# Performance work log

Hardware: AMD Instinct MI355X
Metric: run time of the kernel (lower is better)

Reference implementation:

```python
import jax, jax.numpy as jnp
import numpy as np

H = 1024   # hidden_dim
L = 2      # n_layers
V = 512    # dict_size['target']
B = 256    # batch
S = 512    # encoder seq len
IN = 64    # maxlen['input'][0] = encoder input feature dim
T = 64     # maxlen['target'] = decoder steps


def setup_inputs() -> dict:
    key = jax.random.key(0)
    ks = jax.random.split(key, 16)
    def p(k, shape):
        return jax.random.normal(k, shape, jnp.float32) * 0.05
    emb = p(ks[0], (V, H)).at[0].set(0.0)  # padding_idx=0 row is zero
    return dict(
        x=jax.random.normal(ks[1], (B, S, IN), jnp.float32),
        emb=emb,
        enc_Wih0=p(ks[2], (3 * H, IN)), enc_Whh0=p(ks[3], (3 * H, H)),
        enc_bih0=p(ks[4], (3 * H,)),   enc_bhh0=p(ks[5], (3 * H,)),
        enc_Wih1=p(ks[6], (3 * H, H)), enc_Whh1=p(ks[7], (3 * H, H)),
        enc_bih1=p(ks[8], (3 * H,)),   enc_bhh1=p(ks[9], (3 * H,)),
        dec_Wih=p(ks[10], (L, 3 * H, H)), dec_Whh=p(ks[11], (L, 3 * H, H)),
        dec_bih=p(ks[12], (L, 3 * H)),    dec_bhh=p(ks[13], (L, 3 * H)),
        fc_W=p(ks[14], (V, H)), fc_b=p(ks[15], (V,)),
    )


def gru_cell(x, h, Wih, Whh, bih, bhh):
    # torch GRU cell: r,z,n gate ordering
    gx = x @ Wih.T + bih            # (B, 3H)
    gh = h @ Whh.T + bhh            # (B, 3H)
    rx, zx, nx = jnp.split(gx, 3, axis=-1)
    rh, zh, nh = jnp.split(gh, 3, axis=-1)
    r = jax.nn.sigmoid(rx + rh)
    z = jax.nn.sigmoid(zx + zh)
    n = jnp.tanh(nx + r * nh)
    return (1.0 - z) * n + z * h


def reference(x, emb, enc_Wih0, enc_Whh0, enc_bih0, enc_bhh0,
              enc_Wih1, enc_Whh1, enc_bih1, enc_bhh1,
              dec_Wih, dec_Whh, dec_bih, dec_bhh, fc_W, fc_b):
    b = x.shape[0]
    # ---------- encoder: 2-layer unidirectional GRU ----------
    seq = jnp.swapaxes(x, 0, 1)  # (S, B, IN) time-major for scan
    enc_params = [(enc_Wih0, enc_Whh0, enc_bih0, enc_bhh0),
                  (enc_Wih1, enc_Whh1, enc_bih1, enc_bhh1)]
    finals = []
    for (Wih, Whh, bih, bhh) in enc_params:
        h0 = jnp.zeros((b, H), seq.dtype)
        def step(h, xt, Wih=Wih, Whh=Whh, bih=bih, bhh=bhh):
            hn = gru_cell(xt, h, Wih, Whh, bih, bhh)
            return hn, hn
        hT, seq = jax.lax.scan(step, h0, seq)
        finals.append(hT)
    hidden = jnp.stack(finals)  # (L, B, H)

    tok0 = jnp.zeros((b,), jnp.int32)  # start token 0 (== <pad>)

    def dec_step(carry, _):
        hcur, tok = carry
        inp = emb[tok]                       # (B, H) embedding lookup
        new_h = []
        for l in range(L):
            hn = gru_cell(inp, hcur[l], dec_Wih[l], dec_Whh[l],
                          dec_bih[l], dec_bhh[l])
            new_h.append(hn)
            inp = hn
        logits = inp @ fc_W.T + fc_b         # (B, V)
        tok = jnp.argmax(logits, axis=-1).astype(jnp.int32)
        return (jnp.stack(new_h), tok), logits

    (h_fin, _), logits_seq = jax.lax.scan(dec_step, (hidden, tok0), None, length=T)
    out = jnp.swapaxes(logits_seq, 0, 1)     # (B, T, V)
    return out, h_fin
```

## Files before the change

### kernel.cpp

```cpp
#include <hip/hip_runtime.h>
#include <math.h>

namespace {

constexpr int BSZ = 256;
constexpr int SEQ = 512;
constexpr int KIN = 64;
constexpr int HID = 1024;
constexpr int GD  = 3072;
constexpr int VOC = 512;
constexpr int TT  = 64;

typedef _Float16 half_t;
typedef _Float16 half8 __attribute__((ext_vector_type(8)));
typedef float f32x4 __attribute__((ext_vector_type(4)));

constexpr float LOSCL = 4096.f;
constexpr float LOINV = 1.f / 4096.f;

__device__ __forceinline__ void decode_mc(int bb, int& m0, int& c0) {
  int c_lo = bb & 7, rest = bb >> 3;
  int m = rest & 7, c_hi = rest >> 3;
  m0 = m * 32;
  c0 = (c_hi * 8 + c_lo) * 32;
}

__global__ __launch_bounds__(256) void swz_kernel(
    const float* __restrict__ src, half_t* __restrict__ hi,
    half_t* __restrict__ lo, int NG, int NKCH, int HIDR, int n)
{
  int i = blockIdx.x * 256 + threadIdx.x;
  if (i >= n) return;
  int j = i & 7, l = (i >> 3) & 63;
  int frag = i >> 9;
  int g = frag % NG;
  int rest = frag / NG;
  int w4 = rest & 3;
  int rest2 = rest >> 2;
  int kc = rest2 % NKCH;
  int ct = rest2 / NKCH;
  int ldw = NKCH * 64;
  int row = g * HIDR + ct * 32 + (w4 & 1) * 16 + (l & 15);
  int col = kc * 64 + (w4 >> 1) * 32 + (l >> 4) * 8 + j;
  float f = src[(size_t)row * ldw + col];
  half_t h = (half_t)f;
  hi[i] = h;
  lo[i] = (half_t)((f - (float)h) * LOSCL);
}

typedef half_t AldsT[2][2][32][136];

template<int NG, int G2>
__device__ __forceinline__ void gemm_swz128(
    const float* __restrict__ A, size_t lda, int nch,
    const half_t* __restrict__ Whi, const half_t* __restrict__ Wlo,
    int ct, int kc0, int nkch_tot, int m0,
    f32x4 (&aH)[4][2], f32x4 (&aL)[4][2], AldsT& Alds)
{
  const int tid = threadIdx.x;
  const int wv = tid >> 6, l = tid & 63, lr = l & 15, lk = l >> 4;
  const int colg = wv & 1, ksg = wv >> 1;
  const int arow = tid >> 3, aseg = tid & 7;
  const float* aptr = A + (size_t)(m0 + arow) * lda + aseg * 16;

  const size_t FR = (size_t)NG * 512;
  const size_t S2STR = 2 * FR;
  const size_t CSTR = 8 * FR;
  const size_t bbase =
      (((size_t)(ct * nkch_tot + kc0 + ksg)) * 4 + colg) * FR + l * 8;
  const half_t* bph = Whi + bbase;
  const half_t* bpl = Wlo + bbase;

  float4 paE[4], paO[4];
  half8 bhE[2 * NG], blE[2 * NG], bhO[2 * NG], blO[2 * NG];
  #pragma unroll
  for (int q = 0; q < 4; ++q) paE[q] = *(const float4*)(aptr + q * 4);
  #pragma unroll
  for (int s2 = 0; s2 < 2; ++s2)
    #pragma unroll
    for (int g = 0; g < NG; ++g) {
      bhE[s2 * NG + g] = *(const half8*)(bph + s2 * S2STR + g * 512);
      blE[s2 * NG + g] = *(const half8*)(bpl + s2 * S2STR + g * 512);
    }

#define SWC(pac, bhc, blc, pan, bhn, bln, CH, BUF)                            \
  {                                                                           \
    {               \
      float vals[16] = {pac[0].x, pac[0].y, pac[0].z, pac[0].w,               \
                        pac[1].x, pac[1].y, pac[1].z, pac[1].w,               \
                        pac[2].x, pac[2].y, pac[2].z, pac[2].w,               \
                        pac[3].x, pac[3].y, pac[3].z, pac[3].w};              \
      half8 hi8[2], lo8[2];                                                   \
      _Pragma("unroll") for (int j = 0; j < 16; ++j) {                        \
        float f = vals[j]; half_t h = (half_t)f;                              \
        hi8[j >> 3][j & 7] = h;                                               \
        lo8[j >> 3][j & 7] = (half_t)((f - (float)h) * LOSCL);                \
      }                                                                       \
      *(half8*)&Alds[BUF][0][arow][aseg * 16] = hi8[0];                       \
      *(half8*)&Alds[BUF][0][arow][aseg * 16 + 8] = hi8[1];                   \
      *(half8*)&Alds[BUF][1][arow][aseg * 16] = lo8[0];                       \
      *(half8*)&Alds[BUF][1][arow][aseg * 16 + 8] = lo8[1];                   \
    }                                                                         \
    __syncthreads();                                                          \
    if ((CH) + 1 < nch) {                                                     \
      _Pragma("unroll") for (int q = 0; q < 4; ++q)                           \
        pan[q] = *(const float4*)(aptr + ((CH) + 1) * 128 + q * 4);           \
      _Pragma("unroll") for (int s2 = 0; s2 < 2; ++s2)                        \
        _Pragma("unroll") for (int g = 0; g < NG; ++g) {                      \
          bhn[s2 * NG + g] =                                                  \
              *(const half8*)(bph + ((CH) + 1) * CSTR + s2 * S2STR + g * 512);\
          bln[s2 * NG + g] =                                                  \
              *(const half8*)(bpl + ((CH) + 1) * CSTR + s2 * S2STR + g * 512);\
        }                                                                     \
    }                                                                         \
    _Pragma("unroll") for (int s2 = 0; s2 < 2; ++s2) {                        \
      half8 ah0 = *(const half8*)&Alds[BUF][0][lr][ksg * 64 + s2 * 32 + lk * 8];      \
      half8 ah1 = *(const half8*)&Alds[BUF][0][16 + lr][ksg * 64 + s2 * 32 + lk * 8]; \
      half8 al0 = *(const half8*)&Alds[BUF][1][lr][ksg * 64 + s2 * 32 + lk * 8];      \
      half8 al1 = *(const half8*)&Alds[BUF][1][16 + lr][ksg * 64 + s2 * 32 + lk * 8]; \
      _Pragma("unroll") for (int g = 0; g < NG; ++g) {                        \
        const int slot = (g == 2) ? G2 : g;                                   \
        half8 bh = bhc[s2 * NG + g];                                          \
        half8 bl = blc[s2 * NG + g];                                          \
        aH[slot][0] = __builtin_amdgcn_mfma_f32_16x16x32_f16(ah0, bh, aH[slot][0], 0, 0, 0); \
        aH[slot][1] = __builtin_amdgcn_mfma_f32_16x16x32_f16(ah1, bh, aH[slot][1], 0, 0, 0); \
        aL[slot][0] = __builtin_amdgcn_mfma_f32_16x16x32_f16(ah0, bl, aL[slot][0], 0, 0, 0); \
        aL[slot][0] = __builtin_amdgcn_mfma_f32_16x16x32_f16(al0, bh, aL[slot][0], 0, 0, 0); \
        aL[slot][1] = __builtin_amdgcn_mfma_f32_16x16x32_f16(ah1, bl, aL[slot][1], 0, 0, 0); \
        aL[slot][1] = __builtin_amdgcn_mfma_f32_16x16x32_f16(al1, bh, aL[slot][1], 0, 0, 0); \
      }                                                                       \
    }                                                                         \
  }

  for (int ch = 0; ch < nch; ch += 2) {
    SWC(paE, bhE, blE, paO, bhO, blO, ch, 0)
    SWC(paO, bhO, blO, paE, bhE, blE, (ch + 1), 1)
  }
#undef SWC
}

template<int NG, int G2>
__device__ __forceinline__ void gemm_swz64(
    const float* __restrict__ A, size_t lda,
    const half_t* __restrict__ Whi, const half_t* __restrict__ Wlo,
    int ct, int nkch_tot, int m0,
    f32x4 (&aH)[4][2], f32x4 (&aL)[4][2], AldsT& Alds)
{
  const int tid = threadIdx.x;
  const int wv = tid >> 6, l = tid & 63, lr = l & 15, lk = l >> 4;
  const int colg = wv & 1, ksg = wv >> 1;
  const int arow = tid >> 3, aseg = tid & 7;
  const float* aptr = A + (size_t)(m0 + arow) * lda + aseg * 8;

  const size_t FR = (size_t)NG * 512;
  const size_t bbase =
      (((size_t)(ct * nkch_tot)) * 4 + (colg + 2 * ksg)) * FR + l * 8;
  half8 bh[NG], bl[NG];
  #pragma unroll
  for (int g = 0; g < NG; ++g) {
    bh[g] = *(const half8*)(Whi + bbase + g * 512);
    bl[g] = *(const half8*)(Wlo + bbase + g * 512);
  }
  float4 u0 = *(const float4*)(aptr);
  float4 u1 = *(const float4*)(aptr + 4);
  {
    float vals[8] = {u0.x, u0.y, u0.z, u0.w, u1.x, u1.y, u1.z, u1.w};
    half8 hi8, lo8;
    #pragma unroll
    for (int j = 0; j < 8; ++j) {
      float f = vals[j]; half_t h = (half_t)f;
      hi8[j] = h; lo8[j] = (half_t)((f - (float)h) * LOSCL);
    }
    *(half8*)&Alds[0][0][arow][aseg * 8] = hi8;
    *(half8*)&Alds[0][1][arow][aseg * 8] = lo8;
  }
  __syncthreads();
  half8 ah0 = *(const half8*)&Alds[0][0][lr][ksg * 32 + lk * 8];
  half8 ah1 = *(const half8*)&Alds[0][0][16 + lr][ksg * 32 + lk * 8];
  half8 al0 = *(const half8*)&Alds[0][1][lr][ksg * 32 + lk * 8];
  half8 al1 = *(const half8*)&Alds[0][1][16 + lr][ksg * 32 + lk * 8];
  #pragma unroll
  for (int g = 0; g < NG; ++g) {
    const int slot = (g == 2) ? G2 : g;
    aH[slot][0] = __builtin_amdgcn_mfma_f32_16x16x32_f16(ah0, bh[g], aH[slot][0], 0, 0, 0);
    aH[slot][1] = __builtin_amdgcn_mfma_f32_16x16x32_f16(ah1, bh[g], aH[slot][1], 0, 0, 0);
    aL[slot][0] = __builtin_amdgcn_mfma_f32_16x16x32_f16(ah0, bl[g], aL[slot][0], 0, 0, 0);
    aL[slot][0] = __builtin_amdgcn_mfma_f32_16x16x32_f16(al0, bh[g], aL[slot][0], 0, 0, 0);
    aL[slot][1] = __builtin_amdgcn_mfma_f32_16x16x32_f16(ah1, bl[g], aL[slot][1], 0, 0, 0);
    aL[slot][1] = __builtin_amdgcn_mfma_f32_16x16x32_f16(al1, bh[g], aL[slot][1], 0, 0, 0);
  }
}

template<int NS>
__device__ __forceinline__ void combine_ks(
    f32x4 (&aH)[4][2], f32x4 (&aL)[4][2], float* __restrict__ xch)
{
  const int tid = threadIdx.x;
  const int wv = tid >> 6, l = tid & 63;
  const int colg = wv & 1, ksg = wv >> 1;
  #pragma unroll
  for (int q = 0; q < NS; ++q)
    #pragma unroll
    for (int mf = 0; mf < 2; ++mf)
      aH[q][mf] = aH[q][mf] + aL[q][mf] * LOINV;
  __syncthreads();
  float* base = xch + ((size_t)colg * 64 + l) * (NS * 8);
  if (ksg == 1) {
    #pragma unroll
    for (int q = 0; q < NS; ++q)
      #pragma unroll
      for (int mf = 0; mf < 2; ++mf)
        *(f32x4*)(base + q * 8 + mf * 4) = aH[q][mf];
  }
  __syncthreads();
  if (ksg == 0) {
    #pragma unroll
    for (int q = 0; q < NS; ++q)
      #pragma unroll
      for (int mf = 0; mf < 2; ++mf)
        aH[q][mf] = aH[q][mf] + *(const f32x4*)(base + q * 8 + mf * 4);
  }
}

__device__ __forceinline__ void gru_epi32(
    f32x4 (&vv)[4][2],
    const float* __restrict__ bih, const float* __restrict__ bhh,
    const float* __restrict__ hprev, float* __restrict__ hout,
    int m0, int c0)
{
  const int tid = threadIdx.x;
  if (tid >= 128) return;
  const int wv = tid >> 6, l = tid & 63, lr = l & 15, lk = l >> 4;
  const int c = c0 + (wv & 1) * 16 + lr;
  float bhr = bhh[c], bhz = bhh[HID + c], bhn = bhh[2 * HID + c];
  float bir = 0.f, biz = 0.f, bin = 0.f;
  if (bih) { bir = bih[c]; biz = bih[HID + c]; bin = bih[2 * HID + c]; }
  #pragma unroll
  for (int mf = 0; mf < 2; ++mf) {
    #pragma unroll
    for (int i = 0; i < 4; ++i) {
      int b = m0 + mf * 16 + lk * 4 + i;
      float rs = vv[0][mf][i] + bhr + bir;
      float zs = vv[1][mf][i] + bhz + biz;
      float nx = vv[2][mf][i] + bin;
      float nh = vv[3][mf][i] + bhn;
      float r = 1.f / (1.f + expf(-rs));
      float z = 1.f / (1.f + expf(-zs));
      float n = tanhf(nx + r * nh);
      hout[(size_t)b * HID + c] =
          (1.f - z) * n + z * hprev[(size_t)b * HID + c];
    }
  }
}

__device__ __forceinline__ void write_partials32(
    f32x4 (&vv)[4][2], int s2, float* __restrict__ P, int m0, int c0)
{
  const int tid = threadIdx.x;
  if (tid >= 128) return;
  const int wv = tid >> 6, l = tid & 63, lr = l & 15, lk = l >> 4;
  const int c = c0 + (wv & 1) * 16 + lr;
  #pragma unroll
  for (int g = 0; g < 3; ++g) {
    const int slot = (g == 2) ? s2 : g;
    #pragma unroll
    for (int mf = 0; mf < 2; ++mf) {
      #pragma unroll
      for (int i = 0; i < 4; ++i) {
        int b = m0 + mf * 16 + lk * 4 + i;
        P[((size_t)g * BSZ + b) * HID + c] = vv[slot][mf][i];
      }
    }
  }
}

#define INIT_ACC(aH, aL)                                  \
  _Pragma("unroll") for (int q = 0; q < 4; ++q)           \
    _Pragma("unroll") for (int m_ = 0; m_ < 2; ++m_) {    \
      aH[q][m_] = (f32x4){0.f, 0.f, 0.f, 0.f};            \
      aL[q][m_] = (f32x4){0.f, 0.f, 0.f, 0.f};            \
    }

__global__ __launch_bounds__(256, 2) void enc_step_mfma(
    int s, const float* __restrict__ x,
    const half_t* __restrict__ Wih0h, const half_t* __restrict__ Wih0l,
    const float* __restrict__ bih0,
    const half_t* __restrict__ Whh0h, const half_t* __restrict__ Whh0l,
    const float* __restrict__ bhh0,
    const half_t* __restrict__ Wih1h, const half_t* __restrict__ Wih1l,
    const float* __restrict__ bih1,
    const half_t* __restrict__ Whh1h, const half_t* __restrict__ Whh1l,
    const float* __restrict__ bhh1,
    float* __restrict__ h0f, float* __restrict__ h1f)
{
  __shared__ __align__(16) AldsT Alds;
  f32x4 aH[4][2], aL[4][2];
  INIT_ACC(aH, aL)
  const size_t BH = (size_t)BSZ * HID;
  int blk = blockIdx.x;
  if (blk < 256) {
    if (s >= SEQ) return;
    int m0, c0; decode_mc(blk, m0, c0);
    int ct = c0 >> 5;
    const float* hp = h0f + ((s + 1) & 1) * BH;
    gemm_swz128<3, 3>(hp, HID, 8, Whh0h, Whh0l, ct, 0, 16, m0, aH, aL, Alds);
    gemm_swz64<3, 2>(x + (size_t)s * KIN, (size_t)SEQ * KIN, Wih0h, Wih0l,
                     ct, 1, m0, aH, aL, Alds);
    combine_ks<4>(aH, aL, (float*)Alds);
    gru_epi32(aH, bih0, bhh0, hp, h0f + (s & 1) * BH, m0, c0);
  } else {
    if (s < 1) return;
    int u = s - 1;
    int m0, c0; decode_mc(blk - 256, m0, c0);
    int ct = c0 >> 5;
    const float* hp = h1f + ((u + 1) & 1) * BH;
    const float* h0in = h0f + (u & 1) * BH;
    gemm_swz128<3, 3>(hp, HID, 8, Whh1h, Whh1l, ct, 0, 16, m0, aH, aL, Alds);
    gemm_swz128<3, 2>(h0in, HID, 8, Wih1h, Wih1l, ct, 0, 16, m0, aH, aL, Alds);
    combine_ks<4>(aH, aL, (float*)Alds);
    gru_epi32(aH, bih1, bhh1, hp, h1f + (u & 1) * BH, m0, c0);
  }
}

__global__ __launch_bounds__(256, 2) void gru0_main(
    const float* __restrict__ hprev,
    const half_t* __restrict__ Whhh, const half_t* __restrict__ Whhl,
    float* __restrict__ Pg)
{
  __shared__ __align__(16) AldsT Alds;
  f32x4 aH[4][2], aL[4][2];
  INIT_ACC(aH, aL)
  int bb = blockIdx.x;
  int kh = bb >> 8;
  int m0, c0; decode_mc(bb & 255, m0, c0);
  int ct = c0 >> 5;
  gemm_swz128<3, 3>(hprev + kh * 512, HID, 4, Whhh, Whhl, ct, kh * 8, 16, m0,
                    aH, aL, Alds);
  combine_ks<4>(aH, aL, (float*)Alds);
  write_partials32(aH, 3, Pg + (size_t)kh * 3 * BSZ * HID, m0, c0);
}

__global__ __launch_bounds__(256) void gru0_epi(
    const float* __restrict__ Pg, const float* __restrict__ bhh,
    const float* __restrict__ E, const int* __restrict__ tok,
    const float* __restrict__ hprev, float* __restrict__ hout)
{
  int idx = (blockIdx.x * 256 + threadIdx.x) * 4;
  int b = idx >> 10, c = idx & 1023;
  const size_t BH3 = (size_t)3 * BSZ * HID;
  float4 r0 = *(const float4*)&Pg[((size_t)0 * BSZ + b) * HID + c];
  float4 z0 = *(const float4*)&Pg[((size_t)1 * BSZ + b) * HID + c];
  float4 n0 = *(const float4*)&Pg[((size_t)2 * BSZ + b) * HID + c];
  float4 r1 = *(const float4*)&Pg[BH3 + ((size_t)0 * BSZ + b) * HID + c];
  float4 z1 = *(const float4*)&Pg[BH3 + ((size_t)1 * BSZ + b) * HID + c];
  float4 n1 = *(const float4*)&Pg[BH3 + ((size_t)2 * BSZ + b) * HID + c];
  const float* Er = E + (size_t)tok[b] * GD;
  float4 exr = *(const float4*)&Er[c];
  float4 exz = *(const float4*)&Er[HID + c];
  float4 exn = *(const float4*)&Er[2 * HID + c];
  float4 hp = *(const float4*)&hprev[(size_t)b * HID + c];
  float r0v[4] = {r0.x, r0.y, r0.z, r0.w}, z0v[4] = {z0.x, z0.y, z0.z, z0.w};
  float n0v[4] = {n0.x, n0.y, n0.z, n0.w}, r1v[4] = {r1.x, r1.y, r1.z, r1.w};
  float z1v[4] = {z1.x, z1.y, z1.z, z1.w}, n1v[4] = {n1.x, n1.y, n1.z, n1.w};
  float exrv[4] = {exr.x, exr.y, exr.z, exr.w};
  float exzv[4] = {exz.x, exz.y, exz.z, exz.w};
  float exnv[4] = {exn.x, exn.y, exn.z, exn.w};
  float hpv[4] = {hp.x, hp.y, hp.z, hp.w};
  float ov[4];
  #pragma unroll
  for (int j = 0; j < 4; ++j) {
    int cc = c + j;
    float rs = r0v[j] + r1v[j] + bhh[cc] + exrv[j];
    float zs = z0v[j] + z1v[j] + bhh[HID + cc] + exzv[j];
    float nh = n0v[j] + n1v[j] + bhh[2 * HID + cc];
    float r = 1.f / (1.f + expf(-rs));
    float z = 1.f / (1.f + expf(-zs));
    float n = tanhf(exnv[j] + r * nh);
    ov[j] = (1.f - z) * n + z * hpv[j];
  }
  float4 o; o.x = ov[0]; o.y = ov[1]; o.z = ov[2]; o.w = ov[3];
  *(float4*)&hout[(size_t)b * HID + c] = o;
}

__global__ __launch_bounds__(256, 2) void dec_l1_main(
    const float* __restrict__ hd1prev, const float* __restrict__ ho0,
    const half_t* __restrict__ Whhh, const half_t* __restrict__ Whhl,
    const half_t* __restrict__ Wihh, const half_t* __restrict__ Wihl,
    float* __restrict__ Phh, float* __restrict__ Pih)
{
  __shared__ __align__(16) AldsT Alds;
  f32x4 aH[4][2], aL[4][2];
  INIT_ACC(aH, aL)
  int bb = blockIdx.x;
  if (bb < 256) {
    int m0, c0; decode_mc(bb, m0, c0);
    gemm_swz128<3, 3>(hd1prev, HID, 8, Whhh, Whhl, c0 >> 5, 0, 16, m0,
                      aH, aL, Alds);
    combine_ks<4>(aH, aL, (float*)Alds);
    write_partials32(aH, 3, Phh, m0, c0);
  } else {
    int m0, c0; decode_mc(bb - 256, m0, c0);
    gemm_swz128<3, 2>(ho0, HID, 8, Wihh, Wihl, c0 >> 5, 0, 16, m0,
                      aH, aL, Alds);
    combine_ks<4>(aH, aL, (float*)Alds);
    write_partials32(aH, 2, Pih, m0, c0);
  }
}

__global__ __launch_bounds__(256) void dec_l1_epi(
    const float* __restrict__ Phh, const float* __restrict__ Pih,
    const float* __restrict__ bih, const float* __restrict__ bhh,
    const float* __restrict__ hprev, float* __restrict__ hout)
{
  int idx = (blockIdx.x * 256 + threadIdx.x) * 4;
  int b = idx >> 10, c = idx & 1023;
  float4 rh = *(const float4*)&Phh[((size_t)0 * BSZ + b) * HID + c];
  float4 zh = *(const float4*)&Phh[((size_t)1 * BSZ + b) * HID + c];
  float4 nh = *(const float4*)&Phh[((size_t)2 * BSZ + b) * HID + c];
  float4 rx = *(const float4*)&Pih[((size_t)0 * BSZ + b) * HID + c];
  float4 zx = *(const float4*)&Pih[((size_t)1 * BSZ + b) * HID + c];
  float4 nx = *(const float4*)&Pih[((size_t)2 * BSZ + b) * HID + c];
  float4 hp = *(const float4*)&hprev[(size_t)b * HID + c];
  float rhv[4] = {rh.x, rh.y, rh.z, rh.w}, zhv[4] = {zh.x, zh.y, zh.z, zh.w};
  float nhv[4] = {nh.x, nh.y, nh.z, nh.w}, rxv[4] = {rx.x, rx.y, rx.z, rx.w};
  float zxv[4] = {zx.x, zx.y, zx.z, zx.w}, nxv[4] = {nx.x, nx.y, nx.z, nx.w};
  float hpv[4] = {hp.x, hp.y, hp.z, hp.w};
  float ov[4];
  #pragma unroll
  for (int j = 0; j < 4; ++j) {
    int cc = c + j;
    float r = 1.f / (1.f + expf(-(rhv[j] + rxv[j] + bhh[cc] + bih[cc])));
    float z = 1.f / (1.f + expf(-(zhv[j] + zxv[j] + bhh[HID + cc] + bih[HID + cc])));
    float n = tanhf(nxv[j] + bih[2 * HID + cc] + r * (nhv[j] + bhh[2 * HID + cc]));
    ov[j] = (1.f - z) * n + z * hpv[j];
  }
  float4 o; o.x = ov[0]; o.y = ov[1]; o.z = ov[2]; o.w = ov[3];
  *(float4*)&hout[(size_t)b * HID + c] = o;
}

__global__ __launch_bounds__(256, 2) void fc_main(
    const float* __restrict__ h,
    const half_t* __restrict__ Wh, const half_t* __restrict__ Wl,
    float* __restrict__ Pfc)
{
  __shared__ __align__(16) AldsT Alds;
  f32x4 aH[4][2], aL[4][2];
  INIT_ACC(aH, aL)
  int bb = blockIdx.x;
  int kh = bb >> 7, sub = bb & 127;
  int v_lo = sub & 7, rest = sub >> 3;
  int m = rest & 7, v_hi = rest >> 3;
  int m0 = m * 32, v0 = (v_hi * 8 + v_lo) * 32;
  gemm_swz128<1, 0>(h + kh * 512, HID, 4, Wh, Wl, v0 >> 5, kh * 8, 16, m0,
                    aH, aL, Alds);
  combine_ks<1>(aH, aL, (float*)Alds);

  const int tid = threadIdx.x;
  if (tid >= 128) return;
  const int wv = tid >> 6, l = tid & 63, lr = l & 15, lk = l >> 4;
  int v = v0 + (wv & 1) * 16 + lr;
  float* P = Pfc + (size_t)kh * BSZ * VOC;
  #pragma unroll
  for (int mf = 0; mf < 2; ++mf) {
    #pragma unroll
    for (int i = 0; i < 4; ++i) {
      int b = m0 + mf * 16 + lk * 4 + i;
      P[(size_t)b * VOC + v] = aH[0][mf][i];
    }
  }
}

__global__ __launch_bounds__(256) void fc_epi(
    const float* __restrict__ Pfc, const float* __restrict__ fcb,
    float* __restrict__ out, int t, int* __restrict__ tok)
{
  __shared__ float sv[4];
  __shared__ int si[4];
  int b = blockIdx.x, tid = threadIdx.x;
  int va = tid, vb = tid + 256;
  float lga = Pfc[(size_t)b * VOC + va] + Pfc[((size_t)BSZ + b) * VOC + va] + fcb[va];
  float lgb = Pfc[(size_t)b * VOC + vb] + Pfc[((size_t)BSZ + b) * VOC + vb] + fcb[vb];
  out[((size_t)b * TT + t) * VOC + va] = lga;
  out[((size_t)b * TT + t) * VOC + vb] = lgb;
  float best = lga; int bi = va;
  if (lgb > best) { best = lgb; bi = vb; }
  #pragma unroll
  for (int off = 1; off < 64; off <<= 1) {
    float ov = __shfl_xor(best, off);
    int oi = __shfl_xor(bi, off);
    if (ov > best || (ov == best && oi < bi)) { best = ov; bi = oi; }
  }
  int wv = tid >> 6;
  if ((tid & 63) == 0) { sv[wv] = best; si[wv] = bi; }
  __syncthreads();
  if (tid == 0) {
    #pragma unroll
    for (int w = 1; w < 4; ++w)
      if (sv[w] > best || (sv[w] == best && si[w] < bi)) { best = sv[w]; bi = si[w]; }
    tok[b] = bi;
  }
}

__global__ __launch_bounds__(256) void e0_kernel(
    const float* __restrict__ emb, const float* __restrict__ Wih,
    const float* __restrict__ bih, float* __restrict__ E0)
{
  __shared__ float As[32][34];
  __shared__ float Bs[32][68];
  int m0 = (blockIdx.x & 15) << 5;
  int c0 = (blockIdx.x >> 4) << 6;
  int tid = threadIdx.x, tx = tid & 15, ty = tid >> 4;
  float acc[2][4] = {};
  for (int k0 = 0; k0 < HID; k0 += 32) {
    { int m = tid >> 3, kq = (tid & 7) << 2;
      float4 v = *(const float4*)(emb + (size_t)(m0 + m) * HID + k0 + kq);
      As[kq+0][m] = v.x; As[kq+1][m] = v.y; As[kq+2][m] = v.z; As[kq+3][m] = v.w; }
    #pragma unroll
    for (int r = 0; r < 2; ++r) {
      int idx = (r << 8) + tid;
      int n = idx >> 3, kq = (idx & 7) << 2;
      float4 v = *(const float4*)(Wih + (size_t)(c0 + n) * HID + k0 + kq);
      Bs[kq+0][n] = v.x; Bs[kq+1][n] = v.y; Bs[kq+2][n] = v.z; Bs[kq+3][n] = v.w;
    }
    __syncthreads();
    #pragma unroll 4
    for (int k = 0; k < 32; ++k) {
      float a0 = As[k][(ty << 1)], a1 = As[k][(ty << 1) + 1];
      float4 b = *(const float4*)&Bs[k][tx << 2];
      float bb[4] = {b.x, b.y, b.z, b.w};
      #pragma unroll
      for (int j = 0; j < 4; ++j) {
        acc[0][j] = fmaf(a0, bb[j], acc[0][j]);
        acc[1][j] = fmaf(a1, bb[j], acc[1][j]);
      }
    }
    __syncthreads();
  }
  #pragma unroll
  for (int i = 0; i < 2; ++i) {
    int v = m0 + (ty << 1) + i;
    #pragma unroll
    for (int j = 0; j < 4; ++j) {
      int g = c0 + (tx << 2) + j;
      E0[(size_t)v * GD + g] = acc[i][j] + bih[g];
    }
  }
}

}

extern "C" void kernel_launch(void* const* d_in, const int* in_sizes, int n_in,
                              void* d_out, int out_size, void* d_ws, size_t ws_size,
                              hipStream_t stream)
{
  const float* x     = (const float*)d_in[0];
  const float* emb   = (const float*)d_in[1];
  const float* eWih0 = (const float*)d_in[2];
  const float* eWhh0 = (const float*)d_in[3];
  const float* ebih0 = (const float*)d_in[4];
  const float* ebhh0 = (const float*)d_in[5];
  const float* eWih1 = (const float*)d_in[6];
  const float* eWhh1 = (const float*)d_in[7];
  const float* ebih1 = (const float*)d_in[8];
  const float* ebhh1 = (const float*)d_in[9];
  const float* dWih  = (const float*)d_in[10];
  const float* dWhh  = (const float*)d_in[11];
  const float* dbih  = (const float*)d_in[12];
  const float* dbhh  = (const float*)d_in[13];
  const float* fcW   = (const float*)d_in[14];
  const float* fcb   = (const float*)d_in[15];
  float* out = (float*)d_out;

  const size_t BH = (size_t)BSZ * HID;

  char* p = (char*)d_ws;
  auto alloc = [&](size_t bytes) {
    char* r = p; p += (bytes + 255) & ~(size_t)255; return r;
  };
  float* E0   = (float*)alloc((size_t)VOC * GD * 4);
  float* h0f  = (float*)alloc(2 * BH * 4);
  float* h1f  = (float*)alloc(2 * BH * 4);
  float* hd0f = (float*)alloc(2 * BH * 4);
  float* hd1f = (float*)alloc(2 * BH * 4);
  float* Phh  = (float*)alloc(3 * BH * 4);
  float* Pih  = (float*)alloc(3 * BH * 4);
  float* Pg   = (float*)alloc(6 * BH * 4);
  float* Pfc  = (float*)alloc((size_t)2 * BSZ * VOC * 4);
  const int NW_IH0 = GD * KIN, NW = GD * HID, NW_FC = VOC * HID;
  half_t* eWih0h = (half_t*)alloc((size_t)NW_IH0 * 2);
  half_t* eWih0l = (half_t*)alloc((size_t)NW_IH0 * 2);
  half_t* eWhh0h = (half_t*)alloc((size_t)NW * 2);
  half_t* eWhh0l = (half_t*)alloc((size_t)NW * 2);
  half_t* eWih1h = (half_t*)alloc((size_t)NW * 2);
  half_t* eWih1l = (half_t*)alloc((size_t)NW * 2);
  half_t* eWhh1h = (half_t*)alloc((size_t)NW * 2);
  half_t* eWhh1l = (half_t*)alloc((size_t)NW * 2);
  half_t* dWhh0h = (half_t*)alloc((size_t)NW * 2);
  half_t* dWhh0l = (half_t*)alloc((size_t)NW * 2);
  half_t* dWhh1h = (half_t*)alloc((size_t)NW * 2);
  half_t* dWhh1l = (half_t*)alloc((size_t)NW * 2);
  half_t* dWih1h = (half_t*)alloc((size_t)NW * 2);
  half_t* dWih1l = (half_t*)alloc((size_t)NW * 2);
  half_t* fcWh   = (half_t*)alloc((size_t)NW_FC * 2);
  half_t* fcWl   = (half_t*)alloc((size_t)NW_FC * 2);
  int* tok = (int*)alloc(BSZ * 4);

  hipMemsetAsync(h0f + BH, 0, BH * 4, stream);
  hipMemsetAsync(h1f + BH, 0, BH * 4, stream);
  hipMemsetAsync(tok, 0, BSZ * 4, stream);

  swz_kernel<<<NW_IH0 / 256, 256, 0, stream>>>(eWih0, eWih0h, eWih0l,
                                               3, 1, HID, NW_IH0);
  swz_kernel<<<NW / 256, 256, 0, stream>>>(eWhh0, eWhh0h, eWhh0l,
                                           3, 16, HID, NW);
  swz_kernel<<<NW / 256, 256, 0, stream>>>(eWih1, eWih1h, eWih1l,
                                           3, 16, HID, NW);
  swz_kernel<<<NW / 256, 256, 0, stream>>>(eWhh1, eWhh1h, eWhh1l,
                                           3, 16, HID, NW);
  swz_kernel<<<NW / 256, 256, 0, stream>>>(dWhh, dWhh0h, dWhh0l,
                                           3, 16, HID, NW);
  swz_kernel<<<NW / 256, 256, 0, stream>>>(dWhh + (size_t)NW, dWhh1h, dWhh1l,
                                           3, 16, HID, NW);
  swz_kernel<<<NW / 256, 256, 0, stream>>>(dWih + (size_t)NW, dWih1h, dWih1l,
                                           3, 16, HID, NW);
  swz_kernel<<<NW_FC / 256, 256, 0, stream>>>(fcW, fcWh, fcWl,
                                              1, 16, VOC, NW_FC);

  e0_kernel<<<768, 256, 0, stream>>>(emb, dWih, dbih, E0);

  for (int s = 0; s <= SEQ; ++s) {
    enc_step_mfma<<<512, 256, 0, stream>>>(
        s, x,
        eWih0h, eWih0l, ebih0, eWhh0h, eWhh0l, ebhh0,
        eWih1h, eWih1l, ebih1, eWhh1h, eWhh1l, ebhh1,
        h0f, h1f);
  }

  hipMemcpyAsync(hd0f + BH, h0f + BH, BH * 4, hipMemcpyDeviceToDevice, stream);
  hipMemcpyAsync(hd1f + BH, h1f + BH, BH * 4, hipMemcpyDeviceToDevice, stream);

  for (int t = 0; t < TT; ++t) {
    const float* hp0 = hd0f + ((t + 1) & 1) * BH;
    float* ho0 = hd0f + (t & 1) * BH;
    gru0_main<<<512, 256, 0, stream>>>(hp0, dWhh0h, dWhh0l, Pg);
    gru0_epi<<<256, 256, 0, stream>>>(Pg, dbhh, E0, tok, hp0, ho0);

    const float* hp1 = hd1f + ((t + 1) & 1) * BH;
    float* ho1 = hd1f + (t & 1) * BH;
    dec_l1_main<<<512, 256, 0, stream>>>(hp1, ho0, dWhh1h, dWhh1l,
                                         dWih1h, dWih1l, Phh, Pih);
    dec_l1_epi<<<256, 256, 0, stream>>>(Phh, Pih, dbih + GD, dbhh + GD,
                                        hp1, ho1);
    fc_main<<<256, 256, 0, stream>>>(ho1, fcWh, fcWl, Pfc);
    fc_epi<<<256, 256, 0, stream>>>(Pfc, fcb, out, t, tok);
  }

  hipMemcpyAsync(out + (size_t)BSZ * TT * VOC, hd0f + BH, BH * 4,
                 hipMemcpyDeviceToDevice, stream);
  hipMemcpyAsync(out + (size_t)BSZ * TT * VOC + BH, hd1f + BH, BH * 4,
                 hipMemcpyDeviceToDevice, stream);
}
```

Baseline: 17.14 ms.

## Pre-split activations into fp16 hi/lo in producers and load MFMA operands directly

Each epilogue that produces a hidden state now also writes fp16 hi/lo split copies, and a new kernel pre-splits the encoder input x once. The GEMM routines read those pre-split fp16 A fragments straight from global memory into registers, replacing the per-block fp32 load, convert, LDS staging and __syncthreads. The intent is to remove redundant conversion work and LDS traffic and synchronisation from every recurrent step. In exchange it adds extra global stores per step and uncoalesced-ish direct global fragment loads that may be served less efficiently than LDS.

```diff
diff --git a/kernel.cpp b/kernel.cpp
--- a/kernel.cpp
+++ b/kernel.cpp
@@ -12,6 +12,7 @@
 constexpr int TT  = 64;
 
 typedef _Float16 half_t;
+typedef _Float16 half4 __attribute__((ext_vector_type(4)));
 typedef _Float16 half8 __attribute__((ext_vector_type(8)));
 typedef float f32x4 __attribute__((ext_vector_type(4)));
 
@@ -48,20 +49,39 @@
   lo[i] = (half_t)((f - (float)h) * LOSCL);
 }
 
-typedef half_t AldsT[2][2][32][136];
+__global__ __launch_bounds__(256) void xsplit_kernel(
+    const float* __restrict__ x, half_t* __restrict__ xhi,
+    half_t* __restrict__ xlo, int n4)
+{
+  int i = blockIdx.x * 256 + threadIdx.x;
+  if (i >= n4) return;
+  float4 v = ((const float4*)x)[i];
+  float vv[4] = {v.x, v.y, v.z, v.w};
+  half4 h, lo;
+  #pragma unroll
+  for (int j = 0; j < 4; ++j) {
+    float f = vv[j]; half_t hh = (half_t)f;
+    h[j] = hh; lo[j] = (half_t)((f - (float)hh) * LOSCL);
+  }
+  ((half4*)xhi)[i] = h;
+  ((half4*)xlo)[i] = lo;
+}
 
 template<int NG, int G2>
-__device__ __forceinline__ void gemm_swz128(
-    const float* __restrict__ A, size_t lda, int nch,
+__device__ __forceinline__ void gemm_dir128(
+    const half_t* __restrict__ Ahi, const half_t* __restrict__ Alo,
+    size_t lda, int nch,
     const half_t* __restrict__ Whi, const half_t* __restrict__ Wlo,
     int ct, int kc0, int nkch_tot, int m0,
-    f32x4 (&aH)[4][2], f32x4 (&aL)[4][2], AldsT& Alds)
+    f32x4 (&aH)[4][2], f32x4 (&aL)[4][2])
 {
   const int tid = threadIdx.x;
   const int wv = tid >> 6, l = tid & 63, lr = l & 15, lk = l >> 4;
-  const int colg = wv & 1, ksg = wv >> 1;
-  const int arow = tid >> 3, aseg = tid & 7;
-  const float* aptr = A + (size_t)(m0 + arow) * lda + aseg * 16;
+  const int colg = wv & 1, ksg = (wv >> 1) & 1;
+  const half_t* ah0p = Ahi + (size_t)(m0 + lr) * lda + ksg * 64 + lk * 8;
+  const half_t* ah1p = ah0p + 16 * lda;
+  const half_t* al0p = Alo + (size_t)(m0 + lr) * lda + ksg * 64 + lk * 8;
+  const half_t* al1p = al0p + 16 * lda;
 
   const size_t FR = (size_t)NG * 512;
   const size_t S2STR = 2 * FR;
@@ -71,86 +91,66 @@
   const half_t* bph = Whi + bbase;
   const half_t* bpl = Wlo + bbase;
 
-  float4 paE[4], paO[4];
-  half8 bhE[2 * NG], blE[2 * NG], bhO[2 * NG], blO[2 * NG];
-  #pragma unroll
-  for (int q = 0; q < 4; ++q) paE[q] = *(const float4*)(aptr + q * 4);
-  #pragma unroll
-  for (int s2 = 0; s2 < 2; ++s2)
-    #pragma unroll
-    for (int g = 0; g < NG; ++g) {
-      bhE[s2 * NG + g] = *(const half8*)(bph + s2 * S2STR + g * 512);
-      blE[s2 * NG + g] = *(const half8*)(bpl + s2 * S2STR + g * 512);
-    }
-
-#define SWC(pac, bhc, blc, pan, bhn, bln, CH, BUF)                            \
+  half8 AE[4], AO[4];
+  half8 bhE[NG], blE[NG], bhO[NG], blO[NG];
+  AE[0] = *(const half8*)(ah0p);
+  AE[1] = *(const half8*)(ah1p);
+  AE[2] = *(const half8*)(al0p);
+  AE[3] = *(const half8*)(al1p);
+  #pragma unroll
+  for (int g = 0; g < NG; ++g) {
+    bhE[g] = *(const half8*)(bph + g * 512);
+    blE[g] = *(const half8*)(bpl + g * 512);
+  }
+
+#define DSTG(Ac, bhc, blc, An, bhn, bln, HC)                                  \
   {                                                                           \
-    {               \
-      float vals[16] = {pac[0].x, pac[0].y, pac[0].z, pac[0].w,               \
-                        pac[1].x, pac[1].y, pac[1].z, pac[1].w,               \
-                        pac[2].x, pac[2].y, pac[2].z, pac[2].w,               \
-                        pac[3].x, pac[3].y, pac[3].z, pac[3].w};              \
-      half8 hi8[2], lo8[2];                                                   \
-      _Pragma("unroll") for (int j = 0; j < 16; ++j) {                        \
-        float f = vals[j]; half_t h = (half_t)f;                              \
-        hi8[j >> 3][j & 7] = h;                                               \
-        lo8[j >> 3][j & 7] = (half_t)((f - (float)h) * LOSCL);                \
-      }                                                                       \
-      *(half8*)&Alds[BUF][0][arow][aseg * 16] = hi8[0];                       \
-      *(half8*)&Alds[BUF][0][arow][aseg * 16 + 8] = hi8[1];                   \
-      *(half8*)&Alds[BUF][1][arow][aseg * 16] = lo8[0];                       \
-      *(half8*)&Alds[BUF][1][arow][aseg * 16 + 8] = lo8[1];                   \
-    }                                                                         \
-    __syncthreads();                                                          \
-    if ((CH) + 1 < nch) {                                                     \
-      _Pragma("unroll") for (int q = 0; q < 4; ++q)                           \
-        pan[q] = *(const float4*)(aptr + ((CH) + 1) * 128 + q * 4);           \
-      _Pragma("unroll") for (int s2 = 0; s2 < 2; ++s2)                        \
-        _Pragma("unroll") for (int g = 0; g < NG; ++g) {                      \
-          bhn[s2 * NG + g] =                                                  \
-              *(const half8*)(bph + ((CH) + 1) * CSTR + s2 * S2STR + g * 512);\
-          bln[s2 * NG + g] =                                                  \
-              *(const half8*)(bpl + ((CH) + 1) * CSTR + s2 * S2STR + g * 512);\
-        }                                                                     \
-    }                                                                         \
-    _Pragma("unroll") for (int s2 = 0; s2 < 2; ++s2) {                        \
-      half8 ah0 = *(const half8*)&Alds[BUF][0][lr][ksg * 64 + s2 * 32 + lk * 8];      \
-      half8 ah1 = *(const half8*)&Alds[BUF][0][16 + lr][ksg * 64 + s2 * 32 + lk * 8]; \
-      half8 al0 = *(const half8*)&Alds[BUF][1][lr][ksg * 64 + s2 * 32 + lk * 8];      \
-      half8 al1 = *(const half8*)&Alds[BUF][1][16 + lr][ksg * 64 + s2 * 32 + lk * 8]; \
+    const int nhc = (HC) + 1;                                                 \
+    if (nhc < 2 * nch) {                                                      \
+      const size_t aco = (size_t)(nhc >> 1) * 128 + (size_t)(nhc & 1) * 32;   \
+      const size_t bo = (size_t)(nhc >> 1) * CSTR + (size_t)(nhc & 1) * S2STR;\
+      An[0] = *(const half8*)(ah0p + aco);                                    \
+      An[1] = *(const half8*)(ah1p + aco);                                    \
+      An[2] = *(const half8*)(al0p + aco);                                    \
+      An[3] = *(const half8*)(al1p + aco);                                    \
       _Pragma("unroll") for (int g = 0; g < NG; ++g) {                        \
-        const int slot = (g == 2) ? G2 : g;                                   \
-        half8 bh = bhc[s2 * NG + g];                                          \
-        half8 bl = blc[s2 * NG + g];                                          \
-        aH[slot][0] = __builtin_amdgcn_mfma_f32_16x16x32_f16(ah0, bh, aH[slot][0], 0, 0, 0); \
-        aH[slot][1] = __builtin_amdgcn_mfma_f32_16x16x32_f16(ah1, bh, aH[slot][1], 0, 0, 0); \
-        aL[slot][0] = __builtin_amdgcn_mfma_f32_16x16x32_f16(ah0, bl, aL[slot][0], 0, 0, 0); \
-        aL[slot][0] = __builtin_amdgcn_mfma_f32_16x16x32_f16(al0, bh, aL[slot][0], 0, 0, 0); \
-        aL[slot][1] = __builtin_amdgcn_mfma_f32_16x16x32_f16(ah1, bl, aL[slot][1], 0, 0, 0); \
-        aL[slot][1] = __builtin_amdgcn_mfma_f32_16x16x32_f16(al1, bh, aL[slot][1], 0, 0, 0); \
+        bhn[g] = *(const half8*)(bph + bo + g * 512);                         \
+        bln[g] = *(const half8*)(bpl + bo + g * 512);                         \
       }                                                                       \
     }                                                                         \
-  }
-
-  for (int ch = 0; ch < nch; ch += 2) {
-    SWC(paE, bhE, blE, paO, bhO, blO, ch, 0)
-    SWC(paO, bhO, blO, paE, bhE, blE, (ch + 1), 1)
-  }
-#undef SWC
+    _Pragma("unroll") for (int g = 0; g < NG; ++g) {                          \
+      const int slot = (g == 2) ? G2 : g;                                     \
+      aH[slot][0] = __builtin_amdgcn_mfma_f32_16x16x32_f16(Ac[0], bhc[g], aH[slot][0], 0, 0, 0); \
+      aH[slot][1] = __builtin_amdgcn_mfma_f32_16x16x32_f16(Ac[1], bhc[g], aH[slot][1], 0, 0, 0); \
+      aL[slot][0] = __builtin_amdgcn_mfma_f32_16x16x32_f16(Ac[0], blc[g], aL[slot][0], 0, 0, 0); \
+      aL[slot][0] = __builtin_amdgcn_mfma_f32_16x16x32_f16(Ac[2], bhc[g], aL[slot][0], 0, 0, 0); \
+      aL[slot][1] = __builtin_amdgcn_mfma_f32_16x16x32_f16(Ac[1], blc[g], aL[slot][1], 0, 0, 0); \
+      aL[slot][1] = __builtin_amdgcn_mfma_f32_16x16x32_f16(Ac[3], bhc[g], aL[slot][1], 0, 0, 0); \
+    }                                                                         \
+  }
+
+  for (int hc = 0; hc < 2 * nch; hc += 2) {
+    DSTG(AE, bhE, blE, AO, bhO, blO, hc)
+    DSTG(AO, bhO, blO, AE, bhE, blE, hc + 1)
+  }
+#undef DSTG
 }
 
 template<int NG, int G2>
-__device__ __forceinline__ void gemm_swz64(
-    const float* __restrict__ A, size_t lda,
+__device__ __forceinline__ void gemm_dir64(
+    const half_t* __restrict__ Ahi, const half_t* __restrict__ Alo,
+    size_t lda,
     const half_t* __restrict__ Whi, const half_t* __restrict__ Wlo,
     int ct, int nkch_tot, int m0,
-    f32x4 (&aH)[4][2], f32x4 (&aL)[4][2], AldsT& Alds)
+    f32x4 (&aH)[4][2], f32x4 (&aL)[4][2])
 {
   const int tid = threadIdx.x;
   const int wv = tid >> 6, l = tid & 63, lr = l & 15, lk = l >> 4;
-  const int colg = wv & 1, ksg = wv >> 1;
-  const int arow = tid >> 3, aseg = tid & 7;
-  const float* aptr = A + (size_t)(m0 + arow) * lda + aseg * 8;
+  const int colg = wv & 1, ksg = (wv >> 1) & 1;
+  const half_t* a0 = Ahi + (size_t)(m0 + lr) * lda + ksg * 32 + lk * 8;
+  const half_t* a1 = a0 + 16 * lda;
+  const half_t* c0p = Alo + (size_t)(m0 + lr) * lda + ksg * 32 + lk * 8;
+  const half_t* c1 = c0p + 16 * lda;
 
   const size_t FR = (size_t)NG * 512;
   const size_t bbase =
@@ -161,24 +161,10 @@
     bh[g] = *(const half8*)(Whi + bbase + g * 512);
     bl[g] = *(const half8*)(Wlo + bbase + g * 512);
   }
-  float4 u0 = *(const float4*)(aptr);
-  float4 u1 = *(const float4*)(aptr + 4);
-  {
-    float vals[8] = {u0.x, u0.y, u0.z, u0.w, u1.x, u1.y, u1.z, u1.w};
-    half8 hi8, lo8;
-    #pragma unroll
-    for (int j = 0; j < 8; ++j) {
-      float f = vals[j]; half_t h = (half_t)f;
-      hi8[j] = h; lo8[j] = (half_t)((f - (float)h) * LOSCL);
-    }
-    *(half8*)&Alds[0][0][arow][aseg * 8] = hi8;
-    *(half8*)&Alds[0][1][arow][aseg * 8] = lo8;
-  }
-  __syncthreads();
-  half8 ah0 = *(const half8*)&Alds[0][0][lr][ksg * 32 + lk * 8];
-  half8 ah1 = *(const half8*)&Alds[0][0][16 + lr][ksg * 32 + lk * 8];
-  half8 al0 = *(const half8*)&Alds[0][1][lr][ksg * 32 + lk * 8];
-  half8 al1 = *(const half8*)&Alds[0][1][16 + lr][ksg * 32 + lk * 8];
+  half8 ah0 = *(const half8*)(a0);
+  half8 ah1 = *(const half8*)(a1);
+  half8 al0 = *(const half8*)(c0p);
+  half8 al1 = *(const half8*)(c1);
   #pragma unroll
   for (int g = 0; g < NG; ++g) {
     const int slot = (g == 2) ? G2 : g;
@@ -197,13 +183,12 @@
 {
   const int tid = threadIdx.x;
   const int wv = tid >> 6, l = tid & 63;
-  const int colg = wv & 1, ksg = wv >> 1;
+  const int colg = wv & 1, ksg = (wv >> 1) & 1;
   #pragma unroll
   for (int q = 0; q < NS; ++q)
     #pragma unroll
     for (int mf = 0; mf < 2; ++mf)
       aH[q][mf] = aH[q][mf] + aL[q][mf] * LOINV;
-  __syncthreads();
   float* base = xch + ((size_t)colg * 64 + l) * (NS * 8);
   if (ksg == 1) {
     #pragma unroll
@@ -222,10 +207,11 @@
   }
 }
 
-__device__ __forceinline__ void gru_epi32(
+__device__ __forceinline__ void gru_epi32s(
     f32x4 (&vv)[4][2],
     const float* __restrict__ bih, const float* __restrict__ bhh,
     const float* __restrict__ hprev, float* __restrict__ hout,
+    half_t* __restrict__ houthi, half_t* __restrict__ houtlo,
     int m0, int c0)
 {
   const int tid = threadIdx.x;
@@ -247,8 +233,11 @@
       float r = 1.f / (1.f + expf(-rs));
       float z = 1.f / (1.f + expf(-zs));
       float n = tanhf(nx + r * nh);
-      hout[(size_t)b * HID + c] =
-          (1.f - z) * n + z * hprev[(size_t)b * HID + c];
+      float o = (1.f - z) * n + z * hprev[(size_t)b * HID + c];
+      hout[(size_t)b * HID + c] = o;
+      half_t hv = (half_t)o;
+      houthi[(size_t)b * HID + c] = hv;
+      houtlo[(size_t)b * HID + c] = (half_t)((o - (float)hv) * LOSCL);
     }
   }
 }
@@ -282,7 +271,7 @@
     }
 
 __global__ __launch_bounds__(256, 2) void enc_step_mfma(
-    int s, const float* __restrict__ x,
+    int s, const half_t* __restrict__ xhi, const half_t* __restrict__ xlo,
     const half_t* __restrict__ Wih0h, const half_t* __restrict__ Wih0l,
     const float* __restrict__ bih0,
     const half_t* __restrict__ Whh0h, const half_t* __restrict__ Whh0l,
@@ -291,9 +280,11 @@
     const float* __restrict__ bih1,
     const half_t* __restrict__ Whh1h, const half_t* __restrict__ Whh1l,
     const float* __restrict__ bhh1,
-    float* __restrict__ h0f, float* __restrict__ h1f)
-{
-  __shared__ __align__(16) AldsT Alds;
+    float* __restrict__ h0f, float* __restrict__ h1f,
+    half_t* __restrict__ h0hi, half_t* __restrict__ h0lo,
+    half_t* __restrict__ h1hi, half_t* __restrict__ h1lo)
+{
+  __shared__ __align__(16) float xch[4096];
   f32x4 aH[4][2], aL[4][2];
   INIT_ACC(aH, aL)
   const size_t BH = (size_t)BSZ * HID;
@@ -302,48 +293,53 @@
     if (s >= SEQ) return;
     int m0, c0; decode_mc(blk, m0, c0);
     int ct = c0 >> 5;
-    const float* hp = h0f + ((s + 1) & 1) * BH;
-    gemm_swz128<3, 3>(hp, HID, 8, Whh0h, Whh0l, ct, 0, 16, m0, aH, aL, Alds);
-    gemm_swz64<3, 2>(x + (size_t)s * KIN, (size_t)SEQ * KIN, Wih0h, Wih0l,
-                     ct, 1, m0, aH, aL, Alds);
-    combine_ks<4>(aH, aL, (float*)Alds);
-    gru_epi32(aH, bih0, bhh0, hp, h0f + (s & 1) * BH, m0, c0);
+    const size_t sp = ((s + 1) & 1) * BH, so = (s & 1) * BH;
+    gemm_dir128<3, 3>(h0hi + sp, h0lo + sp, HID, 8, Whh0h, Whh0l,
+                      ct, 0, 16, m0, aH, aL);
+    gemm_dir64<3, 2>(xhi + (size_t)s * KIN, xlo + (size_t)s * KIN,
+                     (size_t)SEQ * KIN, Wih0h, Wih0l, ct, 1, m0, aH, aL);
+    combine_ks<4>(aH, aL, xch);
+    gru_epi32s(aH, bih0, bhh0, h0f + sp, h0f + so, h0hi + so, h0lo + so,
+               m0, c0);
   } else {
     if (s < 1) return;
     int u = s - 1;
     int m0, c0; decode_mc(blk - 256, m0, c0);
     int ct = c0 >> 5;
-    const float* hp = h1f + ((u + 1) & 1) * BH;
-    const float* h0in = h0f + (u & 1) * BH;
-    gemm_swz128<3, 3>(hp, HID, 8, Whh1h, Whh1l, ct, 0, 16, m0, aH, aL, Alds);
-    gemm_swz128<3, 2>(h0in, HID, 8, Wih1h, Wih1l, ct, 0, 16, m0, aH, aL, Alds);
-    combine_ks<4>(aH, aL, (float*)Alds);
-    gru_epi32(aH, bih1, bhh1, hp, h1f + (u & 1) * BH, m0, c0);
+    const size_t up = ((u + 1) & 1) * BH, uo = (u & 1) * BH;
+    gemm_dir128<3, 3>(h1hi + up, h1lo + up, HID, 8, Whh1h, Whh1l,
+                      ct, 0, 16, m0, aH, aL);
+    gemm_dir128<3, 2>(h0hi + uo, h0lo + uo, HID, 8, Wih1h, Wih1l,
+                      ct, 0, 16, m0, aH, aL);
+    combine_ks<4>(aH, aL, xch);
+    gru_epi32s(aH, bih1, bhh1, h1f + up, h1f + uo, h1hi + uo, h1lo + uo,
+               m0, c0);
   }
 }
 
 __global__ __launch_bounds__(256, 2) void gru0_main(
-    const float* __restrict__ hprev,
+    const half_t* __restrict__ hphi, const half_t* __restrict__ hplo,
     const half_t* __restrict__ Whhh, const half_t* __restrict__ Whhl,
     float* __restrict__ Pg)
 {
-  __shared__ __align__(16) AldsT Alds;
+  __shared__ __align__(16) float xch[4096];
   f32x4 aH[4][2], aL[4][2];
   INIT_ACC(aH, aL)
   int bb = blockIdx.x;
   int kh = bb >> 8;
   int m0, c0; decode_mc(bb & 255, m0, c0);
   int ct = c0 >> 5;
-  gemm_swz128<3, 3>(hprev + kh * 512, HID, 4, Whhh, Whhl, ct, kh * 8, 16, m0,
-                    aH, aL, Alds);
-  combine_ks<4>(aH, aL, (float*)Alds);
+  gemm_dir128<3, 3>(hphi + kh * 512, hplo + kh * 512, HID, 4, Whhh, Whhl,
+                    ct, kh * 8, 16, m0, aH, aL);
+  combine_ks<4>(aH, aL, xch);
   write_partials32(aH, 3, Pg + (size_t)kh * 3 * BSZ * HID, m0, c0);
 }
 
 __global__ __launch_bounds__(256) void gru0_epi(
     const float* __restrict__ Pg, const float* __restrict__ bhh,
     const float* __restrict__ E, const int* __restrict__ tok,
-    const float* __restrict__ hprev, float* __restrict__ hout)
+    const float* __restrict__ hprev, float* __restrict__ hout,
+    half_t* __restrict__ houthi, half_t* __restrict__ houtlo)
 {
   int idx = (blockIdx.x * 256 + threadIdx.x) * 4;
   int b = idx >> 10, c = idx & 1023;
@@ -367,6 +363,7 @@
   float exnv[4] = {exn.x, exn.y, exn.z, exn.w};
   float hpv[4] = {hp.x, hp.y, hp.z, hp.w};
   float ov[4];
+  half4 hh, hl;
   #pragma unroll
   for (int j = 0; j < 4; ++j) {
     int cc = c + j;
@@ -377,32 +374,38 @@
     float z = 1.f / (1.f + expf(-zs));
     float n = tanhf(exnv[j] + r * nh);
     ov[j] = (1.f - z) * n + z * hpv[j];
+    half_t hv = (half_t)ov[j];
+    hh[j] = hv;
+    hl[j] = (half_t)((ov[j] - (float)hv) * LOSCL);
   }
   float4 o; o.x = ov[0]; o.y = ov[1]; o.z = ov[2]; o.w = ov[3];
   *(float4*)&hout[(size_t)b * HID + c] = o;
+  *(half4*)&houthi[(size_t)b * HID + c] = hh;
+  *(half4*)&houtlo[(size_t)b * HID + c] = hl;
 }
 
 __global__ __launch_bounds__(256, 2) void dec_l1_main(
-    const float* __restrict__ hd1prev, const float* __restrict__ ho0,
+    const half_t* __restrict__ hd1hi, const half_t* __restrict__ hd1lo,
+    const half_t* __restrict__ ho0hi, const half_t* __restrict__ ho0lo,
     const half_t* __restrict__ Whhh, const half_t* __restrict__ Whhl,
     const half_t* __restrict__ Wihh, const half_t* __restrict__ Wihl,
     float* __restrict__ Phh, float* __restrict__ Pih)
 {
-  __shared__ __align__(16) AldsT Alds;
+  __shared__ __align__(16) float xch[4096];
   f32x4 aH[4][2], aL[4][2];
   INIT_ACC(aH, aL)
   int bb = blockIdx.x;
   if (bb < 256) {
     int m0, c0; decode_mc(bb, m0, c0);
-    gemm_swz128<3, 3>(hd1prev, HID, 8, Whhh, Whhl, c0 >> 5, 0, 16, m0,
-                      aH, aL, Alds);
-    combine_ks<4>(aH, aL, (float*)Alds);
+    gemm_dir128<3, 3>(hd1hi, hd1lo, HID, 8, Whhh, Whhl, c0 >> 5, 0, 16, m0,
+                      aH, aL);
+    combine_ks<4>(aH, aL, xch);
     write_partials32(aH, 3, Phh, m0, c0);
   } else {
     int m0, c0; decode_mc(bb - 256, m0, c0);
-    gemm_swz128<3, 2>(ho0, HID, 8, Wihh, Wihl, c0 >> 5, 0, 16, m0,
-                      aH, aL, Alds);
-    combine_ks<4>(aH, aL, (float*)Alds);
+    gemm_dir128<3, 2>(ho0hi, ho0lo, HID, 8, Wihh, Wihl, c0 >> 5, 0, 16, m0,
+                      aH, aL);
+    combine_ks<4>(aH, aL, xch);
     write_partials32(aH, 2, Pih, m0, c0);
   }
 }
@@ -410,7 +413,8 @@
 __global__ __launch_bounds__(256) void dec_l1_epi(
     const float* __restrict__ Phh, const float* __restrict__ Pih,
     const float* __restrict__ bih, const float* __restrict__ bhh,
-    const float* __restrict__ hprev, float* __restrict__ hout)
+    const float* __restrict__ hprev, float* __restrict__ hout,
+    half_t* __restrict__ houthi, half_t* __restrict__ houtlo)
 {
   int idx = (blockIdx.x * 256 + threadIdx.x) * 4;
   int b = idx >> 10, c = idx & 1023;
@@ -426,6 +430,7 @@
   float zxv[4] = {zx.x, zx.y, zx.z, zx.w}, nxv[4] = {nx.x, nx.y, nx.z, nx.w};
   float hpv[4] = {hp.x, hp.y, hp.z, hp.w};
   float ov[4];
+  half4 hh, hl;
   #pragma unroll
   for (int j = 0; j < 4; ++j) {
     int cc = c + j;
@@ -433,17 +438,22 @@
     float z = 1.f / (1.f + expf(-(zhv[j] + zxv[j] + bhh[HID + cc] + bih[HID + cc])));
     float n = tanhf(nxv[j] + bih[2 * HID + cc] + r * (nhv[j] + bhh[2 * HID + cc]));
     ov[j] = (1.f - z) * n + z * hpv[j];
+    half_t hv = (half_t)ov[j];
+    hh[j] = hv;
+    hl[j] = (half_t)((ov[j] - (float)hv) * LOSCL);
   }
   float4 o; o.x = ov[0]; o.y = ov[1]; o.z = ov[2]; o.w = ov[3];
   *(float4*)&hout[(size_t)b * HID + c] = o;
+  *(half4*)&houthi[(size_t)b * HID + c] = hh;
+  *(half4*)&houtlo[(size_t)b * HID + c] = hl;
 }
 
 __global__ __launch_bounds__(256, 2) void fc_main(
-    const float* __restrict__ h,
+    const half_t* __restrict__ hhi, const half_t* __restrict__ hlo,
     const half_t* __restrict__ Wh, const half_t* __restrict__ Wl,
     float* __restrict__ Pfc)
 {
-  __shared__ __align__(16) AldsT Alds;
+  __shared__ __align__(16) float xch[4096];
   f32x4 aH[4][2], aL[4][2];
   INIT_ACC(aH, aL)
   int bb = blockIdx.x;
@@ -451,9 +461,9 @@
   int v_lo = sub & 7, rest = sub >> 3;
   int m = rest & 7, v_hi = rest >> 3;
   int m0 = m * 32, v0 = (v_hi * 8 + v_lo) * 32;
-  gemm_swz128<1, 0>(h + kh * 512, HID, 4, Wh, Wl, v0 >> 5, kh * 8, 16, m0,
-                    aH, aL, Alds);
-  combine_ks<1>(aH, aL, (float*)Alds);
+  gemm_dir128<1, 0>(hhi + kh * 512, hlo + kh * 512, HID, 4, Wh, Wl,
+                    v0 >> 5, kh * 8, 16, m0, aH, aL);
+  combine_ks<1>(aH, aL, xch);
 
   const int tid = threadIdx.x;
   if (tid >= 128) return;
@@ -572,6 +582,7 @@
   float* out = (float*)d_out;
 
   const size_t BH = (size_t)BSZ * HID;
+  const size_t XN = (size_t)BSZ * SEQ * KIN;
 
   char* p = (char*)d_ws;
   auto alloc = [&](size_t bytes) {
@@ -603,10 +614,24 @@
   half_t* dWih1l = (half_t*)alloc((size_t)NW * 2);
   half_t* fcWh   = (half_t*)alloc((size_t)NW_FC * 2);
   half_t* fcWl   = (half_t*)alloc((size_t)NW_FC * 2);
+  half_t* xhi  = (half_t*)alloc(XN * 2);
+  half_t* xlo  = (half_t*)alloc(XN * 2);
+  half_t* h0hi = (half_t*)alloc(2 * BH * 2);
+  half_t* h0lo = (half_t*)alloc(2 * BH * 2);
+  half_t* h1hi = (half_t*)alloc(2 * BH * 2);
+  half_t* h1lo = (half_t*)alloc(2 * BH * 2);
+  half_t* d0hi = (half_t*)alloc(2 * BH * 2);
+  half_t* d0lo = (half_t*)alloc(2 * BH * 2);
+  half_t* d1hi = (half_t*)alloc(2 * BH * 2);
+  half_t* d1lo = (half_t*)alloc(2 * BH * 2);
   int* tok = (int*)alloc(BSZ * 4);
 
   hipMemsetAsync(h0f + BH, 0, BH * 4, stream);
   hipMemsetAsync(h1f + BH, 0, BH * 4, stream);
+  hipMemsetAsync(h0hi + BH, 0, BH * 2, stream);
+  hipMemsetAsync(h0lo + BH, 0, BH * 2, stream);
+  hipMemsetAsync(h1hi + BH, 0, BH * 2, stream);
+  hipMemsetAsync(h1lo + BH, 0, BH * 2, stream);
   hipMemsetAsync(tok, 0, BSZ * 4, stream);
 
   swz_kernel<<<NW_IH0 / 256, 256, 0, stream>>>(eWih0, eWih0h, eWih0l,
@@ -625,33 +650,41 @@
                                            3, 16, HID, NW);
   swz_kernel<<<NW_FC / 256, 256, 0, stream>>>(fcW, fcWh, fcWl,
                                               1, 16, VOC, NW_FC);
+  xsplit_kernel<<<(int)(XN / 4 / 256), 256, 0, stream>>>(x, xhi, xlo,
+                                                         (int)(XN / 4));
 
   e0_kernel<<<768, 256, 0, stream>>>(emb, dWih, dbih, E0);
 
   for (int s = 0; s <= SEQ; ++s) {
     enc_step_mfma<<<512, 256, 0, stream>>>(
-        s, x,
+        s, xhi, xlo,
         eWih0h, eWih0l, ebih0, eWhh0h, eWhh0l, ebhh0,
         eWih1h, eWih1l, ebih1, eWhh1h, eWhh1l, ebhh1,
-        h0f, h1f);
+        h0f, h1f, h0hi, h0lo, h1hi, h1lo);
   }
 
   hipMemcpyAsync(hd0f + BH, h0f + BH, BH * 4, hipMemcpyDeviceToDevice, stream);
   hipMemcpyAsync(hd1f + BH, h1f + BH, BH * 4, hipMemcpyDeviceToDevice, stream);
+  hipMemcpyAsync(d0hi + BH, h0hi + BH, BH * 2, hipMemcpyDeviceToDevice, stream);
+  hipMemcpyAsync(d0lo + BH, h0lo + BH, BH * 2, hipMemcpyDeviceToDevice, stream);
+  hipMemcpyAsync(d1hi + BH, h1hi + BH, BH * 2, hipMemcpyDeviceToDevice, stream);
+  hipMemcpyAsync(d1lo + BH, h1lo + BH, BH * 2, hipMemcpyDeviceToDevice, stream);
 
   for (int t = 0; t < TT; ++t) {
-    const float* hp0 = hd0f + ((t + 1) & 1) * BH;
-    float* ho0 = hd0f + (t & 1) * BH;
-    gru0_main<<<512, 256, 0, stream>>>(hp0, dWhh0h, dWhh0l, Pg);
-    gru0_epi<<<256, 256, 0, stream>>>(Pg, dbhh, E0, tok, hp0, ho0);
-
-    const float* hp1 = hd1f + ((t + 1) & 1) * BH;
-    float* ho1 = hd1f + (t & 1) * BH;
-    dec_l1_main<<<512, 256, 0, stream>>>(hp1, ho0, dWhh1h, dWhh1l,
-                                         dWih1h, dWih1l, Phh, Pih);
+    const size_t sp = ((t + 1) & 1) * BH, so = (t & 1) * BH;
+    gru0_main<<<512, 256, 0, stream>>>(d0hi + sp, d0lo + sp,
+                                       dWhh0h, dWhh0l, Pg);
+    gru0_epi<<<256, 256, 0, stream>>>(Pg, dbhh, E0, tok, hd0f + sp,
+                                      hd0f + so, d0hi + so, d0lo + so);
+
+    dec_l1_main<<<512, 256, 0, stream>>>(d1hi + sp, d1lo + sp,
+                                         d0hi + so, d0lo + so,
+                                         dWhh1h, dWhh1l, dWih1h, dWih1l,
+                                         Phh, Pih);
     dec_l1_epi<<<256, 256, 0, stream>>>(Phh, Pih, dbih + GD, dbhh + GD,
-                                        hp1, ho1);
-    fc_main<<<256, 256, 0, stream>>>(ho1, fcWh, fcWl, Pfc);
+                                        hd1f + sp, hd1f + so,
+                                        d1hi + so, d1lo + so);
+    fc_main<<<256, 256, 0, stream>>>(d1hi + so, d1lo + so, fcWh, fcWl, Pfc);
     fc_epi<<<256, 256, 0, stream>>>(Pfc, fcb, out, t, tok);
   }
 
```

After: 32.68 ms. +90.6%, slower.
